# Kernel optimization log

Measured on AMD Instinct MI355X. Metric: run time of the kernel, lower is better.

## Reference

```python
import jax, jax.numpy as jnp
import numpy as np

DIM, HEADS, DIM_HEAD = 1024, 16, 64
DIM_INNER = HEADS * DIM_HEAD  # 1024
SCALE = DIM_HEAD ** -0.5


def _rope(t):
    # t: [b, h, n, d]; interleaved-pair RoPE (lucidrains rotary-embedding-torch default)
    d = t.shape[-1]
    n = t.shape[-2]
    inv_freq = 1.0 / (10000.0 ** (jnp.arange(0, d, 2, dtype=jnp.float32) / d))
    angles = jnp.arange(n, dtype=jnp.float32)[:, None] * inv_freq[None, :]  # [n, d/2]
    cos, sin = jnp.cos(angles), jnp.sin(angles)
    t1, t2 = t[..., 0::2], t[..., 1::2]
    r1 = t1 * cos - t2 * sin
    r2 = t1 * sin + t2 * cos
    return jnp.stack([r1, r2], axis=-1).reshape(t.shape)


def setup_inputs() -> dict:
    key = jax.random.key(0)
    ks = jax.random.split(key, 8)
    b, n = 2, 2048
    inp = {
        "x": jax.random.normal(ks[0], (b, n, DIM), dtype=jnp.float32),
        "value_residual": jax.random.normal(ks[1], (b, HEADS, n, DIM_HEAD), dtype=jnp.float32),
        "gamma": jnp.ones((DIM,), dtype=jnp.float32),
        "w_qkv": jax.random.normal(ks[2], (DIM, 3 * DIM_INNER), dtype=jnp.float32) * (DIM ** -0.5),
        "w_mix": jax.random.normal(ks[3], (DIM, HEADS), dtype=jnp.float32) * (DIM ** -0.5),
        "b_mix": jnp.zeros((HEADS,), dtype=jnp.float32),
        "w_gates": jax.random.normal(ks[4], (DIM, HEADS), dtype=jnp.float32) * (DIM ** -0.5),
        "b_gates": jnp.zeros((HEADS,), dtype=jnp.float32),
        "w_out": jax.random.normal(ks[5], (DIM_INNER, DIM), dtype=jnp.float32) * (DIM_INNER ** -0.5),
    }
    return inp


def reference(x, value_residual, gamma, w_qkv, w_mix, b_mix, w_gates, b_gates, w_out):
    b, n, _ = x.shape
    # RMSNorm (lucidrains style: F.normalize * sqrt(dim) * gamma)
    norm = jnp.sqrt(jnp.sum(x * x, axis=-1, keepdims=True))
    xn = x / jnp.maximum(norm, 1e-12) * (DIM ** 0.5) * gamma

    qkv = xn @ w_qkv  # [b, n, 3*h*d]
    qkv = qkv.reshape(b, n, 3, HEADS, DIM_HEAD)
    q, k, v = [jnp.transpose(qkv[:, :, i], (0, 2, 1, 3)) for i in range(3)]  # [b,h,n,d]
    original_values = v

    # learned value-residual lerp
    mix = jax.nn.sigmoid(xn @ w_mix + b_mix)            # [b, n, h]
    mix = jnp.transpose(mix, (0, 2, 1))[..., None]       # [b, h, n, 1]
    v = v * (1.0 - mix) + value_residual * mix

    # rotary on q, k
    q = _rope(q)
    k = _rope(k)

    scores = jnp.einsum("bhid,bhjd->bhij", q, k) * SCALE
    attn = jax.nn.softmax(scores, axis=-1)
    out = jnp.einsum("bhij,bhjd->bhid", attn, v)         # [b, h, n, d]

    gates = jax.nn.sigmoid(xn @ w_gates + b_gates)       # [b, n, h]
    out = out * jnp.transpose(gates, (0, 2, 1))[..., None]

    out = jnp.transpose(out, (0, 2, 1, 3)).reshape(b, n, DIM_INNER)
    return out @ w_out, original_values
```

## Files before the change

### kernel.cpp

```cpp
#include <hip/hip_runtime.h>
#include <hip/hip_bf16.h>
#include <math.h>

#define DIMSZ 1024
#define HEADS 16
#define DHEAD 64
#define NSEQ  2048
#define BATCH 2
#define ROWS  (BATCH*NSEQ)
#define SCALE 0.125f
#define LOG2E 1.4426950408889634f

typedef __attribute__((ext_vector_type(8))) short short8;
typedef __attribute__((ext_vector_type(4))) float floatx4;

#define MFMA16(a,b,c) __builtin_amdgcn_mfma_f32_16x16x32_bf16(a,b,c,0,0,0)

__device__ __forceinline__ void gl2lds16(const void* g, void* l) {
    __builtin_amdgcn_global_load_lds(
        (const __attribute__((address_space(1))) unsigned int*)g,
        (__attribute__((address_space(3))) unsigned int*)l, 16, 0, 0);
}

__device__ __forceinline__ unsigned short bf16r(float a) {
    unsigned u = __float_as_uint(a);
    u += 0x7fff + ((u >> 16) & 1);
    return (unsigned short)(u >> 16);
}
__device__ __forceinline__ unsigned pack_bf16(float a, float b) {
    unsigned ua = __float_as_uint(a), ub = __float_as_uint(b);
    ua += 0x7fff + ((ua >> 16) & 1);
    ub += 0x7fff + ((ub >> 16) & 1);
    return (ua >> 16) | (ub & 0xffff0000u);
}
__device__ __forceinline__ float2 bf2f(unsigned u) {
    float2 r;
    r.x = __uint_as_float(u << 16);
    r.y = __uint_as_float(u & 0xffff0000u);
    return r;
}
__device__ __forceinline__ float fexp2(float x) {
#if __has_builtin(__builtin_amdgcn_exp2f)
    return __builtin_amdgcn_exp2f(x);
#else
    return exp2f(x);
#endif
}
__device__ __forceinline__ float fsin_rev(float x) {
#if __has_builtin(__builtin_amdgcn_sinf)
    return __builtin_amdgcn_sinf(x);
#else
    return __sinf(x * 6.28318530717958647692f);
#endif
}
__device__ __forceinline__ float fcos_rev(float x) {
#if __has_builtin(__builtin_amdgcn_cosf)
    return __builtin_amdgcn_cosf(x);
#else
    return __cosf(x * 6.28318530717958647692f);
#endif
}

__global__ __launch_bounds__(256) void transpose_all_kernel(
    const float* __restrict__ w_qkv, const float* __restrict__ w_out,
    const float* __restrict__ w_mix, const float* __restrict__ w_gates,
    unsigned short* __restrict__ wqkvT, unsigned short* __restrict__ woutT,
    unsigned short* __restrict__ wmgT)
{
    __shared__ float t[32][33];
    const int tx = threadIdx.x & 31, tyy = threadIdx.x >> 5;
    const int bx = blockIdx.x;
    const int k0 = blockIdx.y * 32;
    if (bx < 128) {
        const float* src;
        unsigned short* dst;
        int N, n0;
        if (bx < 96) { src = w_qkv; dst = wqkvT; N = 3*DIMSZ; n0 = bx*32; }
        else         { src = w_out; dst = woutT; N = DIMSZ;   n0 = (bx-96)*32; }
        #pragma unroll
        for (int i = 0; i < 4; i++)
            t[tyy*4 + i][tx] = src[(size_t)(k0 + tyy*4 + i)*N + n0 + tx];
        __syncthreads();
        #pragma unroll
        for (int i = 0; i < 4; i++)
            dst[(size_t)(n0 + tyy*4 + i)*DIMSZ + k0 + tx] = bf16r(t[tx][tyy*4 + i]);
    } else {
        #pragma unroll
        for (int i = 0; i < 4; i++) {
            const int kk = k0 + tyy*4 + i;
            t[tyy*4 + i][tx] = (tx < 16) ? w_mix[kk*16 + tx]
                                         : w_gates[kk*16 + (tx - 16)];
        }
        __syncthreads();
        #pragma unroll
        for (int i = 0; i < 4; i++)
            wmgT[(size_t)(tyy*4 + i)*DIMSZ + k0 + tx] = bf16r(t[tx][tyy*4 + i]);
    }
}

__global__ __launch_bounds__(256) void rmsnorm_kernel(
    const float* __restrict__ x, const float* __restrict__ gamma,
    unsigned short* __restrict__ xnb)
{
    const int row = blockIdx.x;
    const int tid = threadIdx.x;
    __shared__ float wred[4];

    const float4 xv = ((const float4*)(x + (size_t)row * DIMSZ))[tid];
    float ss = xv.x*xv.x + xv.y*xv.y + xv.z*xv.z + xv.w*xv.w;
    #pragma unroll
    for (int off = 1; off < 64; off <<= 1) ss += __shfl_xor(ss, off);
    if ((tid & 63) == 0) wred[tid >> 6] = ss;
    __syncthreads();
    const float total = wred[0] + wred[1] + wred[2] + wred[3];
    const float inv = 32.0f / fmaxf(sqrtf(total), 1e-12f);
    const float4 gv = ((const float4*)gamma)[tid];
    uint2 pk;
    pk.x = pack_bf16(xv.x * inv * gv.x, xv.y * inv * gv.y);
    pk.y = pack_bf16(xv.z * inv * gv.z, xv.w * inv * gv.w);
    ((uint2*)(xnb + (size_t)row * DIMSZ))[tid] = pk;
}

__global__ __launch_bounds__(256) void mix_gates_mfma(
    const unsigned short* __restrict__ A, const unsigned short* __restrict__ WG,
    const float* __restrict__ b_mix, const float* __restrict__ b_gates,
    float* __restrict__ mixo, float* __restrict__ gateso)
{
    __shared__ short As[128*32];
    __shared__ short Bs[32*32];
    const int tid = threadIdx.x;
    const int wv = tid >> 6, lane = tid & 63;
    const int g = lane >> 4, c = lane & 15;
    const int bm = blockIdx.x * 128;

    floatx4 acc[2][2];
    #pragma unroll
    for (int mt = 0; mt < 2; mt++)
        #pragma unroll
        for (int nt = 0; nt < 2; nt++) acc[mt][nt] = (floatx4){0.f,0.f,0.f,0.f};

    for (int k0 = 0; k0 < DIMSZ; k0 += 32) {
        __syncthreads();
        #pragma unroll
        for (int r = 0; r < 2; r++) {
            const int ch = tid + 256*r;
            const int row = ch >> 2, cc = ch & 3;
            gl2lds16(A + (size_t)(bm + row)*DIMSZ + k0 + cc*8, (void*)(As + ch*8));
        }
        if (tid < 128)
            gl2lds16(WG + (size_t)(tid >> 2)*DIMSZ + k0 + (tid & 3)*8, (void*)(Bs + tid*8));
        __syncthreads();
        short8 af[2], bf[2];
        #pragma unroll
        for (int mt = 0; mt < 2; mt++) af[mt] = *(const short8*)(As + (wv*32 + mt*16 + c)*32 + g*8);
        #pragma unroll
        for (int nt = 0; nt < 2; nt++) bf[nt] = *(const short8*)(Bs + (nt*16 + c)*32 + g*8);
        #pragma unroll
        for (int mt = 0; mt < 2; mt++)
            #pragma unroll
            for (int nt = 0; nt < 2; nt++)
                acc[mt][nt] = MFMA16(af[mt], bf[nt], acc[mt][nt]);
    }
    const float bm_c = b_mix[c], bg_c = b_gates[c];
    #pragma unroll
    for (int mt = 0; mt < 2; mt++)
        #pragma unroll
        for (int r2 = 0; r2 < 4; r2++) {
            const int row = bm + wv*32 + mt*16 + g*4 + r2;
            const float lm = acc[mt][0][r2] + bm_c;
            const float lg = acc[mt][1][r2] + bg_c;
            mixo[(size_t)row*HEADS + c]   = 1.0f / (1.0f + fexp2(-lm * LOG2E));
            gateso[(size_t)row*HEADS + c] = 1.0f / (1.0f + fexp2(-lg * LOG2E));
        }
}

__global__ __launch_bounds__(256) void gemm_qkv_mfma(
    const unsigned short* __restrict__ A, const unsigned short* __restrict__ BT,
    unsigned short* __restrict__ qb, unsigned short* __restrict__ kb,
    float* __restrict__ vb)
{
    __shared__ short As[128*32];
    __shared__ short Bs[128*32];
    const int tid = threadIdx.x;
    const int wv = tid >> 6, lane = tid & 63;
    const int g = lane >> 4, c = lane & 15;
    const int wm = wv >> 1, wn = wv & 1;
    const int bm = blockIdx.y * 128, bn = blockIdx.x * 128;

    floatx4 acc[4][4];
    #pragma unroll
    for (int mt = 0; mt < 4; mt++)
        #pragma unroll
        for (int nt = 0; nt < 4; nt++) acc[mt][nt] = (floatx4){0.f,0.f,0.f,0.f};

    for (int k0 = 0; k0 < DIMSZ; k0 += 32) {
        __syncthreads();
        #pragma unroll
        for (int r = 0; r < 2; r++) {
            const int ch = tid + 256*r;
            const int row = ch >> 2, cc = ch & 3;
            gl2lds16(A  + (size_t)(bm + row)*DIMSZ + k0 + cc*8, (void*)(As + ch*8));
            gl2lds16(BT + (size_t)(bn + row)*DIMSZ + k0 + cc*8, (void*)(Bs + ch*8));
        }
        __syncthreads();
        short8 af[4], bf[4];
        #pragma unroll
        for (int mt = 0; mt < 4; mt++) af[mt] = *(const short8*)(As + (wm*64 + mt*16 + c)*32 + g*8);
        #pragma unroll
        for (int nt = 0; nt < 4; nt++) bf[nt] = *(const short8*)(Bs + (wn*64 + nt*16 + c)*32 + g*8);
        #pragma unroll
        for (int mt = 0; mt < 4; mt++)
            #pragma unroll
            for (int nt = 0; nt < 4; nt++)
                acc[mt][nt] = MFMA16(af[mt], bf[nt], acc[mt][nt]);
    }
    __syncthreads();
    const int i3 = bn >> 10;
    const int nb = bn - (i3 << 10);
    if (i3 < 2) {
        unsigned short* dst = (i3 == 0) ? qb : kb;
        short* wbuf = As + wv*1152;
        const int rd_row = lane >> 2, seg = lane & 3;
        #pragma unroll
        for (int mt = 0; mt < 4; mt++) {
            #pragma unroll
            for (int nt = 0; nt < 4; nt++)
                #pragma unroll
                for (int r2 = 0; r2 < 4; r2++)
                    wbuf[(g*4 + r2)*72 + nt*16 + c] = (short)bf16r(acc[mt][nt][r2]);
            __builtin_amdgcn_s_waitcnt(0xc07f);
            const uint4 v0 = *(const uint4*)&wbuf[rd_row*72 + seg*16];
            const uint4 v1 = *(const uint4*)&wbuf[rd_row*72 + seg*16 + 8];
            const int row = bm + wm*64 + mt*16 + rd_row;
            const int col = nb + wn*64 + seg*16;
            const int hh = col >> 6, dd = col & 63;
            const int bb2 = row >> 11, pos = row & 2047;
            unsigned short* dp = dst + (((size_t)(bb2*HEADS + hh)*NSEQ) + pos)*DHEAD + dd;
            *(uint4*)dp = v0;
            *(uint4*)(dp + 8) = v1;
            __builtin_amdgcn_s_waitcnt(0xc07f);
        }
    } else {
        #pragma unroll
        for (int mt = 0; mt < 4; mt++)
            #pragma unroll
            for (int nt = 0; nt < 4; nt++)
                #pragma unroll
                for (int r2 = 0; r2 < 4; r2++) {
                    const int row = bm + wm*64 + mt*16 + g*4 + r2;
                    const int col = nb + wn*64 + nt*16 + c;
                    const int hh = col >> 6, dd = col & 63;
                    const int bb2 = row >> 11, pos = row & 2047;
                    vb[(((size_t)(bb2*HEADS + hh)*NSEQ) + pos)*DHEAD + dd] = acc[mt][nt][r2];
                }
    }
}

__global__ __launch_bounds__(256) void rope_blend_kernel2(
    unsigned short* __restrict__ q, unsigned short* __restrict__ k,
    const float* __restrict__ vorig, const float* __restrict__ vres,
    const float* __restrict__ mixb, unsigned short* __restrict__ vT)
{
    __shared__ unsigned short vt[64*72];
    const int tid = threadIdx.x;
    const int bh = blockIdx.y, bb = bh >> 4, h = bh & 15;
    const int p0 = blockIdx.x * 64;
    {
        const int pr = tid >> 2, d0 = (tid & 3) * 16;
        const int pos = p0 + pr;
        const size_t base = ((size_t)bh*NSEQ + pos)*DHEAD + d0;

        uint4 qr0 = *(uint4*)(q + base), qr1 = *(uint4*)(q + base + 8);
        uint4 kr0 = *(uint4*)(k + base), kr1 = *(uint4*)(k + base + 8);
        unsigned qw[8] = {qr0.x, qr0.y, qr0.z, qr0.w, qr1.x, qr1.y, qr1.z, qr1.w};
        unsigned kw[8] = {kr0.x, kr0.y, kr0.z, kr0.w, kr1.x, kr1.y, kr1.z, kr1.w};
        const float QSC = SCALE * LOG2E;
        const float posf = (float)pos;
        #pragma unroll
        for (int j = 0; j < 8; j++) {
            const float pf = (float)((d0 >> 1) + j);
            const float rev = posf * fexp2(-pf * 0.41524101186092029f
                                           - 2.6514961294723187f);
            const float rf = rev - floorf(rev);
            const float sn = fsin_rev(rf);
            const float cs = fcos_rev(rf);
            float2 qv = bf2f(qw[j]);
            float2 kv = bf2f(kw[j]);
            const float q1 = qv.x*cs - qv.y*sn, q2 = qv.x*sn + qv.y*cs;
            const float k1 = kv.x*cs - kv.y*sn, k2 = kv.x*sn + kv.y*cs;
            qw[j] = pack_bf16(q1*QSC, q2*QSC);
            kw[j] = pack_bf16(k1, k2);
        }
        *(uint4*)(q + base)     = *(uint4*)(qw + 0);
        *(uint4*)(q + base + 8) = *(uint4*)(qw + 4);
        *(uint4*)(k + base)     = *(uint4*)(kw + 0);
        *(uint4*)(k + base + 8) = *(uint4*)(kw + 4);

        float vv[16], vr[16];
        #pragma unroll
        for (int i = 0; i < 4; i++) {
            *(float4*)(vv + i*4) = *(const float4*)(vorig + base + i*4);
            *(float4*)(vr + i*4) = *(const float4*)(vres + base + i*4);
        }
        const float mx = mixb[((size_t)(bb*NSEQ + pos))*HEADS + h];
        #pragma unroll
        for (int j = 0; j < 8; j++) {
            const float b0 = vv[2*j]*(1.f-mx)   + vr[2*j]*mx;
            const float b1 = vv[2*j+1]*(1.f-mx) + vr[2*j+1]*mx;
            vt[pr*72 + d0 + 2*j]     = bf16r(b0);
            vt[pr*72 + d0 + 2*j + 1] = bf16r(b1);
        }
    }
    __syncthreads();
    {
        const int dd = tid >> 2, c0 = (tid & 3) * 16;
        unsigned o[8];
        #pragma unroll
        for (int j = 0; j < 8; j++) {
            const unsigned a  = vt[(c0 + 2*j)*72 + dd];
            const unsigned b2 = vt[(c0 + 2*j + 1)*72 + dd];
            o[j] = a | (b2 << 16);
        }
        unsigned short* dst = vT + ((size_t)bh*DHEAD + dd)*NSEQ + p0 + c0;
        *(uint4*)(dst)     = *(uint4*)(o + 0);
        *(uint4*)(dst + 8) = *(uint4*)(o + 4);
    }
}

__global__ __launch_bounds__(256, 4) void attn_mfma_kernel(
    const unsigned short* __restrict__ qg,
    const unsigned short* __restrict__ kg,
    const unsigned short* __restrict__ vT,
    unsigned short* __restrict__ Op0,
    unsigned short* __restrict__ Op1,
    float* __restrict__ lpart)
{
    __shared__ short Kt[2][64*64];
    __shared__ short Vt[2][64*64];
    __shared__ short Ps[4*16*64];

    const int tid = threadIdx.x;
    const int w = tid >> 6, lane = tid & 63;
    const int g = lane >> 4, c = lane & 15;

    int wg = blockIdx.y * gridDim.x + blockIdx.x;
    wg = (wg & 7) * 128 + (wg >> 3);
    const int q0 = (wg & 15) * 128;
    const int byy = wg >> 4;
    const int bh = byy >> 1, s = byy & 1;
    const int bb = bh >> 4, h = bh & 15;

    short8 qf[2][2];
    #pragma unroll
    for (int mt = 0; mt < 2; mt++)
        #pragma unroll
        for (int kb = 0; kb < 2; kb++)
            qf[mt][kb] = *(const short8*)(qg + ((size_t)bh*NSEQ + q0 + w*32 + mt*16 + c)*DHEAD + kb*32 + g*8);

    floatx4 O[2][4];
    #pragma unroll
    for (int mt = 0; mt < 2; mt++)
        #pragma unroll
        for (int nt = 0; nt < 4; nt++) O[mt][nt] = (floatx4){0.f,0.f,0.f,0.f};
    float lsum[2] = {0.f, 0.f};

    short* PsW = Ps + w * 1024;
    const unsigned short* kbase = kg + (size_t)bh*NSEQ*DHEAD;
    const unsigned short* vbase = vT + (size_t)bh*DHEAD*NSEQ;

    {
        const int kt = s*16;
        #pragma unroll
        for (int r = 0; r < 2; r++) {
            const int ch = tid + 256*r;
            const int row = ch >> 3;
            const int u = (ch & 7) ^ (row & 7);
            gl2lds16(kbase + (size_t)(kt*64 + row)*DHEAD + u*8, (void*)(&Kt[0][0] + ch*8));
            gl2lds16(vbase + (size_t)row*NSEQ + kt*64 + u*8,   (void*)(&Vt[0][0] + ch*8));
        }
    }
    __syncthreads();

    for (int i = 0; i < 16; i++) {
        const int cur = i & 1;
        const short* Ktc = &Kt[cur][0];
        const short* Vtc = &Vt[cur][0];

        if (i < 15) {
            const int kt = s*16 + i + 1;
            short* Ktn = &Kt[cur ^ 1][0];
            short* Vtn = &Vt[cur ^ 1][0];
            #pragma unroll
            for (int r = 0; r < 2; r++) {
                const int ch = tid + 256*r;
                const int row = ch >> 3;
                const int u = (ch & 7) ^ (row & 7);
                gl2lds16(kbase + (size_t)(kt*64 + row)*DHEAD + u*8, (void*)(Ktn + ch*8));
                gl2lds16(vbase + (size_t)row*NSEQ + kt*64 + u*8,   (void*)(Vtn + ch*8));
            }
        }

        short8 kfr[4][2];
        #pragma unroll
        for (int nt = 0; nt < 4; nt++) {
            const int rowk = nt*16 + c;
            #pragma unroll
            for (int kb = 0; kb < 2; kb++)
                kfr[nt][kb] = *(const short8*)(Ktc + rowk*64 + (((kb*4 + g) ^ (rowk & 7)) * 8));
        }

        #pragma unroll
        for (int mt = 0; mt < 2; mt++) {
            #pragma unroll
            for (int nt = 0; nt < 4; nt++) {
                floatx4 accS = (floatx4){0.f,0.f,0.f,0.f};
                __builtin_amdgcn_s_setprio(1);
                accS = MFMA16(kfr[nt][0], qf[mt][0], accS);
                accS = MFMA16(kfr[nt][1], qf[mt][1], accS);
                __builtin_amdgcn_s_setprio(0);
                const float p0 = fexp2(accS[0]);
                const float p1 = fexp2(accS[1]);
                const float p2 = fexp2(accS[2]);
                const float p3 = fexp2(accS[3]);
                lsum[mt] += (p0 + p1) + (p2 + p3);
                uint2 pk;
                pk.x = pack_bf16(p0, p1);
                pk.y = pack_bf16(p2, p3);
                *(uint2*)(PsW + c*64 + (((nt*2 + (g >> 1)) ^ (c & 7)) * 8) + (g & 1)*4) = pk;
            }
            __builtin_amdgcn_s_waitcnt(0xc07f);
            __builtin_amdgcn_s_setprio(1);
            #pragma unroll
            for (int kb = 0; kb < 2; kb++) {
                short8 pf = *(const short8*)(PsW + c*64 + (((kb*4 + g) ^ (c & 7)) * 8));
                #pragma unroll
                for (int nt = 0; nt < 4; nt++) {
                    const int rv = nt*16 + c;
                    short8 vf = *(const short8*)(Vtc + rv*64 + (((kb*4 + g) ^ (rv & 7)) * 8));
                    O[mt][nt] = MFMA16(pf, vf, O[mt][nt]);
                }
            }
            __builtin_amdgcn_s_setprio(0);
        }
        __syncthreads();
    }

    unsigned short* Op = s ? Op1 : Op0;
    #pragma unroll
    for (int mt = 0; mt < 2; mt++) {
        float l = lsum[mt];
        l += __shfl_xor(l, 16);
        l += __shfl_xor(l, 32);
        if (g == 0) {
            const int rowl = q0 + w*32 + mt*16 + c;
            lpart[((size_t)s*ROWS + bb*NSEQ + rowl)*HEADS + h] = l;
        }
        #pragma unroll
        for (int r2 = 0; r2 < 4; r2++) {
            const int rowg = q0 + w*32 + mt*16 + g*4 + r2;
            unsigned short* op = Op + ((size_t)(bb*NSEQ + rowg))*DIMSZ + h*DHEAD + c;
            #pragma unroll
            for (int nt = 0; nt < 4; nt++)
                op[nt*16] = bf16r(O[mt][nt][r2]);
        }
    }
}

__global__ __launch_bounds__(256) void attn_combine_kernel(
    const unsigned short* __restrict__ Op1, const float* __restrict__ lpart,
    const float* __restrict__ gates, unsigned short* __restrict__ attnO)
{
    const int idx = blockIdx.x * 256 + threadIdx.x;
    const int row = idx >> 7;
    const int c8 = (idx & 127) * 8;
    const int h = c8 >> 6;
    const float l0 = lpart[(size_t)row*HEADS + h];
    const float l1 = lpart[((size_t)ROWS + row)*HEADS + h];
    const float gt = gates[(size_t)row*HEADS + h];
    const float sc = gt / (l0 + l1);
    const size_t base = (size_t)row*DIMSZ + c8;
    const uint4 a = *(const uint4*)(attnO + base);
    const uint4 b = *(const uint4*)(Op1 + base);
    const unsigned aw[4] = {a.x, a.y, a.z, a.w};
    const unsigned bw[4] = {b.x, b.y, b.z, b.w};
    unsigned o[4];
    #pragma unroll
    for (int j = 0; j < 4; j++) {
        const float2 fa = bf2f(aw[j]);
        const float2 fb = bf2f(bw[j]);
        o[j] = pack_bf16((fa.x + fb.x)*sc, (fa.y + fb.y)*sc);
    }
    *(uint4*)(attnO + base) = *(uint4*)o;
}

__global__ __launch_bounds__(256) void gemm_out_mfma(
    const unsigned short* __restrict__ A, const unsigned short* __restrict__ BT,
    float* __restrict__ out0)
{
    __shared__ short As[128*32];
    __shared__ short Bs[128*32];
    const int tid = threadIdx.x;
    const int wv = tid >> 6, lane = tid & 63;
    const int g = lane >> 4, c = lane & 15;
    const int wm = wv >> 1, wn = wv & 1;
    const int bm = blockIdx.y * 128, bn = blockIdx.x * 128;

    floatx4 acc[4][4];
    #pragma unroll
    for (int mt = 0; mt < 4; mt++)
        #pragma unroll
        for (int nt = 0; nt < 4; nt++) acc[mt][nt] = (floatx4){0.f,0.f,0.f,0.f};

    for (int k0 = 0; k0 < DIMSZ; k0 += 32) {
        __syncthreads();
        #pragma unroll
        for (int r = 0; r < 2; r++) {
            const int ch = tid + 256*r;
            const int row = ch >> 2, cc = ch & 3;
            gl2lds16(A  + (size_t)(bm + row)*DIMSZ + k0 + cc*8, (void*)(As + ch*8));
            gl2lds16(BT + (size_t)(bn + row)*DIMSZ + k0 + cc*8, (void*)(Bs + ch*8));
        }
        __syncthreads();
        short8 af[4], bf[4];
        #pragma unroll
        for (int mt = 0; mt < 4; mt++) af[mt] = *(const short8*)(As + (wm*64 + mt*16 + c)*32 + g*8);
        #pragma unroll
        for (int nt = 0; nt < 4; nt++) bf[nt] = *(const short8*)(Bs + (wn*64 + nt*16 + c)*32 + g*8);
        #pragma unroll
        for (int mt = 0; mt < 4; mt++)
            #pragma unroll
            for (int nt = 0; nt < 4; nt++)
                acc[mt][nt] = MFMA16(af[mt], bf[nt], acc[mt][nt]);
    }
    #pragma unroll
    for (int mt = 0; mt < 4; mt++)
        #pragma unroll
        for (int nt = 0; nt < 4; nt++)
            #pragma unroll
            for (int r2 = 0; r2 < 4; r2++) {
                const int row = bm + wm*64 + mt*16 + g*4 + r2;
                const int col = bn + wn*64 + nt*16 + c;
                out0[(size_t)row*DIMSZ + col] = acc[mt][nt][r2];
            }
}

extern "C" void kernel_launch(void* const* d_in, const int* in_sizes, int n_in,
                              void* d_out, int out_size, void* d_ws, size_t ws_size,
                              hipStream_t stream) {
    const float* x       = (const float*)d_in[0];
    const float* vres    = (const float*)d_in[1];
    const float* gamma   = (const float*)d_in[2];
    const float* w_qkv   = (const float*)d_in[3];
    const float* w_mix   = (const float*)d_in[4];
    const float* b_mix   = (const float*)d_in[5];
    const float* w_gates = (const float*)d_in[6];
    const float* b_gates = (const float*)d_in[7];
    const float* w_out   = (const float*)d_in[8];

    float* out0 = (float*)d_out;
    float* out1 = out0 + (size_t)ROWS * DIMSZ;

    char* ws = (char*)d_ws;
    unsigned short* xnb   = (unsigned short*)(ws);
    unsigned short* wqkvT = (unsigned short*)(ws + (8u<<20));
    unsigned short* woutT = (unsigned short*)(ws + (14u<<20));
    unsigned short* qb2   = (unsigned short*)(ws + (16u<<20));
    unsigned short* kb2   = (unsigned short*)(ws + (24u<<20));
    unsigned short* vT    = (unsigned short*)(ws + (32u<<20));
    unsigned short* attnO = (unsigned short*)(ws + (40u<<20));
    float*          mixb  = (float*)(ws + (48u<<20));
    float*          gatesb= (float*)(ws + (48u<<20) + 262144);
    unsigned short* wmgT  = (unsigned short*)(ws + (49u<<20));
    unsigned short* Op1   = (unsigned short*)(ws + (50u<<20));
    float*          lpart = (float*)(ws + (58u<<20));

    transpose_all_kernel<<<dim3(129, DIMSZ/32), 256, 0, stream>>>(
        w_qkv, w_out, w_mix, w_gates, wqkvT, woutT, wmgT);

    rmsnorm_kernel<<<ROWS, 256, 0, stream>>>(x, gamma, xnb);

    mix_gates_mfma<<<ROWS/128, 256, 0, stream>>>(
        xnb, wmgT, b_mix, b_gates, mixb, gatesb);

    gemm_qkv_mfma<<<dim3(3*DIMSZ/128, ROWS/128), 256, 0, stream>>>(
        xnb, wqkvT, qb2, kb2, out1);

    rope_blend_kernel2<<<dim3(NSEQ/64, BATCH*HEADS), 256, 0, stream>>>(
        qb2, kb2, out1, vres, mixb, vT);

    attn_mfma_kernel<<<dim3(NSEQ/128, BATCH*HEADS*2), 256, 0, stream>>>(
        qb2, kb2, vT, attnO, Op1, lpart);

    attn_combine_kernel<<<ROWS*DIMSZ/8/256, 256, 0, stream>>>(
        Op1, lpart, gatesb, attnO);

    gemm_out_mfma<<<dim3(DIMSZ/128, ROWS/128), 256, 0, stream>>>(
        attnO, woutT, out0);
}
```

Before: 263.1 us.

## Use 32x32 MFMA in attention and keep P in registers via permlane swap

Rewrites the attention inner loop to use 32x32x16 bf16 MFMA tiles instead of 16x16x32. The exponentiated scores are converted with v_cvt_pk_bf16_f32 and redistributed across lanes with permlane32_swap, so they feed the PV MFMA directly. This removes the LDS round-trip for P and its waitcnt. The risks are higher register pressure from the 16-wide accumulators under launch_bounds(256,4), and possible LDS bank conflicts in the new K/V read pattern.

Result: faster. 249.3 us (-5.2%).

```diff
diff --git a/kernel.cpp b/kernel.cpp
--- a/kernel.cpp
+++ b/kernel.cpp
@@ -13,8 +13,11 @@
 
 typedef __attribute__((ext_vector_type(8))) short short8;
 typedef __attribute__((ext_vector_type(4))) float floatx4;
+typedef __attribute__((ext_vector_type(16))) float floatx16;
+typedef __attribute__((ext_vector_type(4))) unsigned uintx4;
 
 #define MFMA16(a,b,c) __builtin_amdgcn_mfma_f32_16x16x32_bf16(a,b,c,0,0,0)
+#define MFMA32(a,b,c) __builtin_amdgcn_mfma_f32_32x32x16_bf16(a,b,c,0,0,0)
 
 __device__ __forceinline__ void gl2lds16(const void* g, void* l) {
     __builtin_amdgcn_global_load_lds(
@@ -38,6 +41,19 @@
     r.x = __uint_as_float(u << 16);
     r.y = __uint_as_float(u & 0xffff0000u);
     return r;
+}
+__device__ __forceinline__ unsigned cvtpk(float lo, float hi) {
+    unsigned r;
+    asm("v_cvt_pk_bf16_f32 %0, %1, %2" : "=v"(r) : "v"(lo), "v"(hi));
+    return r;
+}
+__device__ __forceinline__ void pl32swap(unsigned &a, unsigned &b) {
+#if __has_builtin(__builtin_amdgcn_permlane32_swap)
+    auto r = __builtin_amdgcn_permlane32_swap(a, b, false, false);
+    a = (unsigned)r[0]; b = (unsigned)r[1];
+#else
+    asm volatile("v_permlane32_swap_b32 %0, %1" : "+v"(a), "+v"(b));
+#endif
 }
 __device__ __forceinline__ float fexp2(float x) {
 #if __has_builtin(__builtin_amdgcn_exp2f)
@@ -337,11 +353,10 @@
 {
     __shared__ short Kt[2][64*64];
     __shared__ short Vt[2][64*64];
-    __shared__ short Ps[4*16*64];
 
     const int tid = threadIdx.x;
     const int w = tid >> 6, lane = tid & 63;
-    const int g = lane >> 4, c = lane & 15;
+    const int hi = lane >> 5, cq = lane & 31;
 
     int wg = blockIdx.y * gridDim.x + blockIdx.x;
     wg = (wg & 7) * 128 + (wg >> 3);
@@ -350,21 +365,14 @@
     const int bh = byy >> 1, s = byy & 1;
     const int bb = bh >> 4, h = bh & 15;
 
-    short8 qf[2][2];
-    #pragma unroll
-    for (int mt = 0; mt < 2; mt++)
-        #pragma unroll
-        for (int kb = 0; kb < 2; kb++)
-            qf[mt][kb] = *(const short8*)(qg + ((size_t)bh*NSEQ + q0 + w*32 + mt*16 + c)*DHEAD + kb*32 + g*8);
-
-    floatx4 O[2][4];
-    #pragma unroll
-    for (int mt = 0; mt < 2; mt++)
-        #pragma unroll
-        for (int nt = 0; nt < 4; nt++) O[mt][nt] = (floatx4){0.f,0.f,0.f,0.f};
-    float lsum[2] = {0.f, 0.f};
-
-    short* PsW = Ps + w * 1024;
+    short8 qf[4];
+    #pragma unroll
+    for (int kd = 0; kd < 4; kd++)
+        qf[kd] = *(const short8*)(qg + ((size_t)bh*NSEQ + q0 + w*32 + cq)*DHEAD + kd*16 + hi*8);
+
+    floatx16 O0{}, O1{};
+    float lsum = 0.f;
+
     const unsigned short* kbase = kg + (size_t)bh*NSEQ*DHEAD;
     const unsigned short* vbase = vT + (size_t)bh*DHEAD*NSEQ;
 
@@ -400,44 +408,54 @@
             }
         }
 
-        short8 kfr[4][2];
-        #pragma unroll
-        for (int nt = 0; nt < 4; nt++) {
-            const int rowk = nt*16 + c;
-            #pragma unroll
-            for (int kb = 0; kb < 2; kb++)
-                kfr[nt][kb] = *(const short8*)(Ktc + rowk*64 + (((kb*4 + g) ^ (rowk & 7)) * 8));
-        }
-
-        #pragma unroll
-        for (int mt = 0; mt < 2; mt++) {
-            #pragma unroll
-            for (int nt = 0; nt < 4; nt++) {
-                floatx4 accS = (floatx4){0.f,0.f,0.f,0.f};
-                __builtin_amdgcn_s_setprio(1);
-                accS = MFMA16(kfr[nt][0], qf[mt][0], accS);
-                accS = MFMA16(kfr[nt][1], qf[mt][1], accS);
-                __builtin_amdgcn_s_setprio(0);
-                const float p0 = fexp2(accS[0]);
-                const float p1 = fexp2(accS[1]);
-                const float p2 = fexp2(accS[2]);
-                const float p3 = fexp2(accS[3]);
-                lsum[mt] += (p0 + p1) + (p2 + p3);
-                uint2 pk;
-                pk.x = pack_bf16(p0, p1);
-                pk.y = pack_bf16(p2, p3);
-                *(uint2*)(PsW + c*64 + (((nt*2 + (g >> 1)) ^ (c & 7)) * 8) + (g & 1)*4) = pk;
+        #pragma unroll
+        for (int kt2 = 0; kt2 < 2; kt2++) {
+            floatx16 accS{};
+            const int rowk = kt2*32 + cq;
+            __builtin_amdgcn_s_setprio(1);
+            #pragma unroll
+            for (int kd = 0; kd < 4; kd++) {
+                short8 kf = *(const short8*)(Ktc + rowk*64 + (((kd*2 + hi) ^ (cq & 7)) * 8));
+                accS = MFMA32(kf, qf[kd], accS);
             }
-            __builtin_amdgcn_s_waitcnt(0xc07f);
+            __builtin_amdgcn_s_setprio(0);
+
+            float p[16];
+            #pragma unroll
+            for (int r = 0; r < 16; r++) p[r] = fexp2(accS[r]);
+            const float a1 = (p[0]+p[1]) + (p[2]+p[3]);
+            const float a2 = (p[4]+p[5]) + (p[6]+p[7]);
+            const float a3 = (p[8]+p[9]) + (p[10]+p[11]);
+            const float a4 = (p[12]+p[13]) + (p[14]+p[15]);
+            lsum += (a1+a2) + (a3+a4);
+
+            unsigned d0 = cvtpk(p[0],  p[1]);
+            unsigned d1 = cvtpk(p[2],  p[3]);
+            unsigned d2 = cvtpk(p[4],  p[5]);
+            unsigned d3 = cvtpk(p[6],  p[7]);
+            unsigned d4 = cvtpk(p[8],  p[9]);
+            unsigned d5 = cvtpk(p[10], p[11]);
+            unsigned d6 = cvtpk(p[12], p[13]);
+            unsigned d7 = cvtpk(p[14], p[15]);
+            pl32swap(d0, d2);
+            pl32swap(d1, d3);
+            pl32swap(d4, d6);
+            pl32swap(d5, d7);
+            const uintx4 t0 = {d0, d1, d2, d3};
+            const uintx4 t1 = {d4, d5, d6, d7};
+            const short8 pf0 = __builtin_bit_cast(short8, t0);
+            const short8 pf1 = __builtin_bit_cast(short8, t1);
+
             __builtin_amdgcn_s_setprio(1);
             #pragma unroll
-            for (int kb = 0; kb < 2; kb++) {
-                short8 pf = *(const short8*)(PsW + c*64 + (((kb*4 + g) ^ (c & 7)) * 8));
+            for (int ks2 = 0; ks2 < 2; ks2++) {
+                const short8 pf = ks2 ? pf1 : pf0;
                 #pragma unroll
-                for (int nt = 0; nt < 4; nt++) {
-                    const int rv = nt*16 + c;
-                    short8 vf = *(const short8*)(Vtc + rv*64 + (((kb*4 + g) ^ (rv & 7)) * 8));
-                    O[mt][nt] = MFMA16(pf, vf, O[mt][nt]);
+                for (int nt2 = 0; nt2 < 2; nt2++) {
+                    const int rv = nt2*32 + cq;
+                    short8 vf = *(const short8*)(Vtc + rv*64 + (((kt2*4 + ks2*2 + hi) ^ (cq & 7)) * 8));
+                    if (nt2 == 0) O0 = MFMA32(pf, vf, O0);
+                    else          O1 = MFMA32(pf, vf, O1);
                 }
             }
             __builtin_amdgcn_s_setprio(0);
@@ -446,23 +464,16 @@
     }
 
     unsigned short* Op = s ? Op1 : Op0;
-    #pragma unroll
-    for (int mt = 0; mt < 2; mt++) {
-        float l = lsum[mt];
-        l += __shfl_xor(l, 16);
-        l += __shfl_xor(l, 32);
-        if (g == 0) {
-            const int rowl = q0 + w*32 + mt*16 + c;
-            lpart[((size_t)s*ROWS + bb*NSEQ + rowl)*HEADS + h] = l;
-        }
-        #pragma unroll
-        for (int r2 = 0; r2 < 4; r2++) {
-            const int rowg = q0 + w*32 + mt*16 + g*4 + r2;
-            unsigned short* op = Op + ((size_t)(bb*NSEQ + rowg))*DIMSZ + h*DHEAD + c;
-            #pragma unroll
-            for (int nt = 0; nt < 4; nt++)
-                op[nt*16] = bf16r(O[mt][nt][r2]);
-        }
+    float l = lsum + __shfl_xor(lsum, 32);
+    if (hi == 0)
+        lpart[((size_t)s*ROWS + bb*NSEQ + q0 + w*32 + cq)*HEADS + h] = l;
+    #pragma unroll
+    for (int reg = 0; reg < 16; reg++) {
+        const int qq = (reg & 3) + 8*(reg >> 2) + 4*hi;
+        const int rowg = q0 + w*32 + qq;
+        unsigned short* op = Op + ((size_t)(bb*NSEQ + rowg))*DIMSZ + h*DHEAD + cq;
+        op[0]  = bf16r(O0[reg]);
+        op[32] = bf16r(O1[reg]);
     }
 }
 
```
